# Kernel tuning notes

Hardware: AMD Instinct MI355X
Metric: run time of the kernel (lower is better)

The kernel has to match this reference:

```python
import jax, jax.numpy as jnp
import numpy as np

B, DIM, T = 8, 1024, 2048
K, CS = 8, 512            # num_codebooks, codebook_size
CHUNK = DIM // K          # 128
TEMP = 1.0                # temp buffer (temp_init, eval-time constant)
EPS = 1e-10


def setup_inputs() -> dict:
    key = jax.random.key(0)
    k1, k2, k3, k4, k5 = jax.random.split(key, 5)
    fan_in = CHUNK
    scale = 1.0 / np.sqrt(fan_in)
    return {
        "x": jax.random.normal(k1, (B, DIM, T), dtype=jnp.float32),
        "proj_w": jax.random.normal(k2, (K, CS, CHUNK), dtype=jnp.float32) * scale,
        "proj_b": jax.random.normal(k3, (K, CS), dtype=jnp.float32) * 0.01,
        "codebooks": jax.random.normal(k4, (K, CS, CHUNK), dtype=jnp.float32) * scale,
        "uniform_noise": jax.random.uniform(k5, (B, K, CS, T), dtype=jnp.float32),
    }


def reference(x, proj_w, proj_b, codebooks, uniform_noise):
    b, d, t = x.shape
    # split channels into per-codebook chunks: [B, K, CHUNK, T]
    xc = x.reshape(b, K, CHUNK, t)
    # 1x1 conv per codebook == per-position matmul: [B, K, CS, T]
    logits = jnp.einsum('bkct,koc->bkot', xc, proj_w) + proj_b[None, :, :, None]
    # gumbel noise from uniform samples
    g = -jnp.log(-jnp.log(uniform_noise + EPS) + EPS)
    # softmax over codebook-entry axis (axis=2), matching F.gumbel_softmax on transposed logits
    soft = jax.nn.softmax((logits + g) / TEMP, axis=2)
    # hard one-hot with straight-through estimator
    idx = jnp.argmax(soft, axis=2)                             # [B, K, T]
    hard = jax.nn.one_hot(idx, CS, axis=2, dtype=soft.dtype)   # [B, K, CS, T]
    onehot = hard + soft - jax.lax.stop_gradient(soft)
    # perplexity per codebook from mean usage over (batch, time)
    avg_probs = onehot.mean(axis=(0, 3))                       # [K, CS]
    perplexity = jnp.exp(jnp.nansum(-avg_probs * jnp.log(avg_probs + 1e-8), axis=1))
    # differentiable codebook gather: [B, K, CHUNK, T] -> [B, DIM, T]
    quantized = jnp.einsum('bkct,kcd->bkdt', onehot, codebooks).reshape(b, d, t)
    return quantized, perplexity
```

## Files before the change

### kernel.cpp

```cpp
#include <hip/hip_runtime.h>
#include <cmath>

#define B 8
#define DIM 1024
#define T 2048
#define K 8
#define CS 512
#define CHUNK 128
#define TT 128
#define TPL 2
#define NW 8
#define OPW 64
#define OG 8
#define NG (OPW / OG)
#define EPS 1e-10f

__global__ __launch_bounds__(512, 2) void gumbel_fused_kernel(
    const float* __restrict__ x,
    const float* __restrict__ proj_w,
    const float* __restrict__ proj_b,
    const float* __restrict__ codebooks,
    const float* __restrict__ noise,
    float* __restrict__ out,
    unsigned int* __restrict__ counts)
{
    __shared__ float Xs[CHUNK * TT];
    __shared__ float redv[NW][TT];
    __shared__ int   redi[NW][TT];

    const int tid = threadIdx.x;
    const int nt = T / TT;
    const int t0 = (blockIdx.x % nt) * TT;
    const int bk = blockIdx.x / nt;
    const int k = bk % K;

    {
        const float* xb = x + (size_t)bk * CHUNK * T + t0;
        const int nv = CHUNK * TT / 4;
        for (int i = tid; i < nv; i += 512) {
            const int row = i >> 5;
            const int c4 = (i & 31) << 2;
            *(float4*)(&Xs[row * TT + c4]) = *(const float4*)(xb + (size_t)row * T + c4);
        }
    }
    __syncthreads();

    const int w = __builtin_amdgcn_readfirstlane(tid >> 6);
    const int lane = tid & 63;
    const int tl = lane * TPL;

    const float* wb = proj_w + ((size_t)k * CS + w * OPW) * CHUNK;
    const float* bb = proj_b + (size_t)k * CS + w * OPW;
    const float* nb = noise + ((size_t)bk * CS + w * OPW) * T + t0 + tl;

    float bv0 = -INFINITY, bv1 = -INFINITY;
    int bi0 = 0, bi1 = 0;

    for (int og = 0; og < NG; ++og) {
        float acc[OG][TPL];
#pragma unroll
        for (int oo = 0; oo < OG; ++oo) { acc[oo][0] = 0.f; acc[oo][1] = 0.f; }

        const float* wrow = wb + (size_t)(og * OG) * CHUNK;
        for (int cb = 0; cb < CHUNK; cb += 4) {
            float2 xv[4];
#pragma unroll
            for (int j = 0; j < 4; ++j)
                xv[j] = *(const float2*)(&Xs[(cb + j) * TT + tl]);
#pragma unroll
            for (int oo = 0; oo < OG; ++oo) {
                const float* wr = wrow + oo * CHUNK + cb;
#pragma unroll
                for (int j = 0; j < 4; ++j) {
                    acc[oo][0] = fmaf(wr[j], xv[j].x, acc[oo][0]);
                    acc[oo][1] = fmaf(wr[j], xv[j].y, acc[oo][1]);
                }
            }
        }

#pragma unroll
        for (int oo = 0; oo < OG; ++oo) {
            const int o = og * OG + oo;
            const float bias = bb[o];
            const float2 u = *(const float2*)(nb + (size_t)o * T);
            const float g0 = -logf(-logf(u.x + EPS) + EPS);
            const float g1 = -logf(-logf(u.y + EPS) + EPS);
            const float l0 = acc[oo][0] + bias + g0;
            const float l1 = acc[oo][1] + bias + g1;
            const int oi = w * OPW + o;
            if (l0 > bv0) { bv0 = l0; bi0 = oi; }
            if (l1 > bv1) { bv1 = l1; bi1 = oi; }
        }
    }

    redv[w][tl] = bv0; redv[w][tl + 1] = bv1;
    redi[w][tl] = bi0; redi[w][tl + 1] = bi1;
    __syncthreads();

    if (tid < TT) {
        float best = redv[0][tid];
        int besti = redi[0][tid];
#pragma unroll
        for (int ww = 1; ww < NW; ++ww) {
            if (redv[ww][tid] > best) { best = redv[ww][tid]; besti = redi[ww][tid]; }
        }
        redi[0][tid] = besti;
        atomicAdd(&counts[k * CS + besti], 1u);
    }
    __syncthreads();

    {
        const int t = tid & (TT - 1);
        const int cq = tid >> 7;
        const int row = redi[0][t];
        const float* crow = codebooks + ((size_t)k * CS + row) * CHUNK + cq * 32;
        float* ob = out + (size_t)bk * CHUNK * T + t0 + t;
#pragma unroll
        for (int i = 0; i < 8; ++i) {
            const float4 v = *(const float4*)(crow + i * 4);
            const int c = cq * 32 + i * 4;
            ob[(size_t)(c + 0) * T] = v.x;
            ob[(size_t)(c + 1) * T] = v.y;
            ob[(size_t)(c + 2) * T] = v.z;
            ob[(size_t)(c + 3) * T] = v.w;
        }
    }
}

__global__ void perplexity_kernel(const unsigned int* __restrict__ counts,
                                  float* __restrict__ out)
{
    const int k = threadIdx.x >> 6;
    const int lane = threadIdx.x & 63;
    float sum = 0.0f;
    const float inv_bt = 1.0f / (float)(B * T);
#pragma unroll
    for (int i = lane; i < CS; i += 64) {
        const float avg = (float)counts[k * CS + i] * inv_bt;
        sum += -avg * logf(avg + 1e-8f);
    }
#pragma unroll
    for (int off = 32; off > 0; off >>= 1) sum += __shfl_down(sum, off, 64);
    if (lane == 0) out[(size_t)B * DIM * T + k] = expf(sum);
}

extern "C" void kernel_launch(void* const* d_in, const int* in_sizes, int n_in,
                              void* d_out, int out_size, void* d_ws, size_t ws_size,
                              hipStream_t stream) {
    const float* x         = (const float*)d_in[0];
    const float* proj_w    = (const float*)d_in[1];
    const float* proj_b    = (const float*)d_in[2];
    const float* codebooks = (const float*)d_in[3];
    const float* noise     = (const float*)d_in[4];
    float* out             = (float*)d_out;
    unsigned int* counts   = (unsigned int*)d_ws;

    hipMemsetAsync(counts, 0, (size_t)K * CS * sizeof(unsigned int), stream);

    const int nblocks = B * K * (T / TT);
    gumbel_fused_kernel<<<nblocks, 512, 0, stream>>>(
        x, proj_w, proj_b, codebooks, noise, out, counts);

    perplexity_kernel<<<1, 512, 0, stream>>>(counts, out);
}
```

Measured before the change: 640.9 us.

## Double-buffer projection weight loads in registers and raise occupancy target

Replaces the wave-uniform scalar weight loads with per-lane float4 vector loads that are software-pipelined: the next 4-column weight slice is fetched into a second register set while the current one feeds the FMAs. It also removes readfirstlane from the wave index, disables unrolling of the outer loops, and raises the launch_bounds occupancy hint from 2 to 4 blocks per CU. The aim is to hide global weight-load latency behind compute. In exchange, weights now go through vector loads and registers instead of scalar loads, and the occupancy hint may force register spills.

```diff
diff --git a/kernel.cpp b/kernel.cpp
--- a/kernel.cpp
+++ b/kernel.cpp
@@ -15,7 +15,7 @@
 #define NG (OPW / OG)
 #define EPS 1e-10f
 
-__global__ __launch_bounds__(512, 2) void gumbel_fused_kernel(
+__global__ __launch_bounds__(512, 4) void gumbel_fused_kernel(
     const float* __restrict__ x,
     const float* __restrict__ proj_w,
     const float* __restrict__ proj_b,
@@ -45,7 +45,7 @@
     }
     __syncthreads();
 
-    const int w = __builtin_amdgcn_readfirstlane(tid >> 6);
+    const int w = tid >> 6;
     const int lane = tid & 63;
     const int tl = lane * TPL;
 
@@ -56,24 +56,64 @@
     float bv0 = -INFINITY, bv1 = -INFINITY;
     int bi0 = 0, bi1 = 0;
 
+    float4 wv[OG], wn[OG];
+#pragma unroll
+    for (int oo = 0; oo < OG; ++oo)
+        wv[oo] = *(const float4*)(wb + (size_t)oo * CHUNK);
+
+#pragma unroll 1
     for (int og = 0; og < NG; ++og) {
         float acc[OG][TPL];
 #pragma unroll
         for (int oo = 0; oo < OG; ++oo) { acc[oo][0] = 0.f; acc[oo][1] = 0.f; }
 
         const float* wrow = wb + (size_t)(og * OG) * CHUNK;
-        for (int cb = 0; cb < CHUNK; cb += 4) {
-            float2 xv[4];
-#pragma unroll
-            for (int j = 0; j < 4; ++j)
-                xv[j] = *(const float2*)(&Xs[(cb + j) * TT + tl]);
-#pragma unroll
-            for (int oo = 0; oo < OG; ++oo) {
-                const float* wr = wrow + oo * CHUNK + cb;
-#pragma unroll
-                for (int j = 0; j < 4; ++j) {
-                    acc[oo][0] = fmaf(wr[j], xv[j].x, acc[oo][0]);
-                    acc[oo][1] = fmaf(wr[j], xv[j].y, acc[oo][1]);
+
+#pragma unroll 1
+        for (int cb = 0; cb < CHUNK; cb += 8) {
+            {
+                const float* pr = wrow + cb + 4;
+#pragma unroll
+                for (int oo = 0; oo < OG; ++oo)
+                    wn[oo] = *(const float4*)(pr + (size_t)oo * CHUNK);
+
+                float2 xv[4];
+#pragma unroll
+                for (int j = 0; j < 4; ++j)
+                    xv[j] = *(const float2*)(&Xs[(cb + j) * TT + tl]);
+#pragma unroll
+                for (int oo = 0; oo < OG; ++oo) {
+                    acc[oo][0] = fmaf(wv[oo].x, xv[0].x, acc[oo][0]);
+                    acc[oo][1] = fmaf(wv[oo].x, xv[0].y, acc[oo][1]);
+                    acc[oo][0] = fmaf(wv[oo].y, xv[1].x, acc[oo][0]);
+                    acc[oo][1] = fmaf(wv[oo].y, xv[1].y, acc[oo][1]);
+                    acc[oo][0] = fmaf(wv[oo].z, xv[2].x, acc[oo][0]);
+                    acc[oo][1] = fmaf(wv[oo].z, xv[2].y, acc[oo][1]);
+                    acc[oo][0] = fmaf(wv[oo].w, xv[3].x, acc[oo][0]);
+                    acc[oo][1] = fmaf(wv[oo].w, xv[3].y, acc[oo][1]);
+                }
+            }
+            {
+                const float* pr = (cb + 8 < CHUNK) ? (wrow + cb + 8)
+                                : ((og + 1 < NG) ? (wrow + (size_t)OG * CHUNK) : wb);
+#pragma unroll
+                for (int oo = 0; oo < OG; ++oo)
+                    wv[oo] = *(const float4*)(pr + (size_t)oo * CHUNK);
+
+                float2 xv[4];
+#pragma unroll
+                for (int j = 0; j < 4; ++j)
+                    xv[j] = *(const float2*)(&Xs[(cb + 4 + j) * TT + tl]);
+#pragma unroll
+                for (int oo = 0; oo < OG; ++oo) {
+                    acc[oo][0] = fmaf(wn[oo].x, xv[0].x, acc[oo][0]);
+                    acc[oo][1] = fmaf(wn[oo].x, xv[0].y, acc[oo][1]);
+                    acc[oo][0] = fmaf(wn[oo].y, xv[1].x, acc[oo][0]);
+                    acc[oo][1] = fmaf(wn[oo].y, xv[1].y, acc[oo][1]);
+                    acc[oo][0] = fmaf(wn[oo].z, xv[2].x, acc[oo][0]);
+                    acc[oo][1] = fmaf(wn[oo].z, xv[2].y, acc[oo][1]);
+                    acc[oo][0] = fmaf(wn[oo].w, xv[3].x, acc[oo][0]);
+                    acc[oo][1] = fmaf(wn[oo].w, xv[3].y, acc[oo][1]);
                 }
             }
         }
```

New measurement: 1.126 ms. 1.76x slower.
